# Kernel optimization log

Hardware: AMD Instinct MI355X
Metric: run time of the kernel (lower is better)

## Reference

```python
import jax, jax.numpy as jnp
import numpy as np

EPSILON = 0.3
ALPHA = 0.7
LN_EPS = 1e-5


def _layernorm(x, g, b):
    mu = jnp.mean(x, axis=-1, keepdims=True)
    var = jnp.mean((x - mu) ** 2, axis=-1, keepdims=True)
    return (x - mu) / jnp.sqrt(var + LN_EPS) * g + b


def setup_inputs() -> dict:
    key = jax.random.key(0)
    ks = jax.random.split(key, 6)
    B, N, D, L = 1, 2048, 768, 16
    s = 0.05  # weight scale to keep sigmoid/exp well-conditioned
    return {
        "x": jax.random.normal(ks[0], (B, N, D), jnp.float32),
        "proj_w": jax.random.normal(ks[1], (D, L), jnp.float32) * s,
        "proj_b": jnp.zeros((L,), jnp.float32),
        "ln1_g": jnp.ones((L,), jnp.float32),
        "ln1_b": jnp.zeros((L,), jnp.float32),
        "pi_w1": jax.random.normal(ks[2], (L, D), jnp.float32) * s,
        "pi_b1": jnp.zeros((D,), jnp.float32),
        "pi_w2": jax.random.normal(ks[3], (D, 1), jnp.float32) * s,
        "pi_b2": jnp.zeros((1,), jnp.float32),
        "dt": jnp.full((1,), 0.05, jnp.float32),
        "f_w": jax.random.normal(ks[4], (D, D), jnp.float32) * s,
        "f_b": jnp.zeros((D,), jnp.float32),
        "ln2_g": jnp.ones((D,), jnp.float32),
        "ln2_b": jnp.zeros((D,), jnp.float32),
    }


def reference(x, proj_w, proj_b, ln1_g, ln1_b, pi_w1, pi_b1, pi_w2, pi_b2, dt, f_w, f_b, ln2_g, ln2_b):
    B, N, D = x.shape
    # proj_list: Linear -> LayerNorm -> ReLU. [B,N,L]
    x_proj = jax.nn.relu(_layernorm(x @ proj_w + proj_b, ln1_g, ln1_b))
    # RBF kernel over pairwise differences. [B,N,N]
    diff = x_proj[:, :, None, :] - x_proj[:, None, :, :]
    K_eps = jnp.exp(-(1.0 / (4.0 * EPSILON)) * jnp.sum(diff * diff, axis=-1))
    q_tilde = jnp.sum(K_eps, axis=2)  # [B,N]
    # pi_list: Linear -> ReLU -> Linear -> Sigmoid. [B,N]
    pi = jax.nn.sigmoid(jax.nn.relu(x_proj @ pi_w1 + pi_b1) @ pi_w2 + pi_b2)[..., 0]
    v = pi / q_tilde  # diagonal of D_epsilon_tilde
    # K_tilde = K_eps @ diag(v): column scaling (math-equivalent to bmm with diag_embed)
    K_tilde = K_eps * v[:, None, :]
    d = jnp.sum(K_tilde, axis=2) + 1e-5  # diagonal of D_tilde
    # inv(D_tilde) @ K_tilde: row scaling; then subtract identity
    L_op = (1.0 / EPSILON) * (K_tilde / d[:, :, None]) - jnp.eye(N, dtype=x.dtype)[None]
    L_mat = L_op[0]  # .squeeze(0), B == 1
    # f(x): modeled as linear map
    target = x @ f_w + f_b  # [B,N,D]
    tt = dt * jnp.einsum('ij,bjd->bid', L_mat, target)  # target_transformed
    target1 = target + tt
    target2 = ALPHA * x + (1.0 - ALPHA) * (target1 + tt)
    return _layernorm(target2, ln2_g, ln2_b)
```

## Files before the change

### kernel.cpp

```cpp
#include <hip/hip_runtime.h>
#include <math.h>

#define EPSILON 0.3f
#define ALPHA 0.7f
#define LN_EPS 1e-5f

typedef __bf16 bf16x8 __attribute__((ext_vector_type(8)));
typedef float f32x4 __attribute__((ext_vector_type(4)));

__device__ __forceinline__ unsigned short f2bf(float f) {
  unsigned int u = __float_as_uint(f);
  return (unsigned short)((u + 0x7fffu + ((u >> 16) & 1u)) >> 16);
}
__device__ __forceinline__ unsigned int pack2(float lo, float hi) {
  return (unsigned int)f2bf(lo) | ((unsigned int)f2bf(hi) << 16);
}

__device__ __forceinline__ float wave_reduce(float v) {
#pragma unroll
  for (int off = 32; off > 0; off >>= 1) v += __shfl_xor(v, off, 64);
  return v;
}

__device__ __forceinline__ float blk_reduce_sum(float v, float* red) {
  v = wave_reduce(v);
  int lane = threadIdx.x & 63, wid = threadIdx.x >> 6;
  __syncthreads();
  if (lane == 0) red[wid] = v;
  __syncthreads();
  float s = 0.f;
  int nw = (blockDim.x + 63) >> 6;
  for (int w = 0; w < nw; ++w) s += red[w];
  return s;
}

__global__ __launch_bounds__(256) void k_proj(
    const float* __restrict__ x, const float* __restrict__ proj_w,
    const float* __restrict__ proj_b, const float* __restrict__ ln1_g,
    const float* __restrict__ ln1_b, const float* __restrict__ pi_w1,
    const float* __restrict__ pi_b1, const float* __restrict__ pi_w2,
    const float* __restrict__ pi_b2, float* __restrict__ xp,
    float* __restrict__ s, float* __restrict__ pi, int N, int D) {
  __shared__ float xs[16][68];
  __shared__ float ws[64][20];
  __shared__ float ysh[16][17];
  __shared__ float xps[16][16];
  __shared__ float pr[16][4];
  int tid = threadIdx.x;
  int row0 = blockIdx.x * 16;
  int row = tid >> 4, l = tid & 15;
  int lane = tid & 63, w = tid >> 6;
  int skc = (tid & 15) * 4;
  int wk = tid >> 2, wl = (tid & 3) * 4;
  float acc = 0.f;
  for (int k0 = 0; k0 < D; k0 += 64) {
    float4 xv = *(const float4*)(x + (size_t)(row0 + row) * D + k0 + skc);
    float4 wv = *(const float4*)(proj_w + (size_t)(k0 + wk) * 16 + wl);
    __syncthreads();
    *(float4*)&xs[row][skc] = xv;
    *(float4*)&ws[wk][wl] = wv;
    __syncthreads();
#pragma unroll
    for (int kk = 0; kk < 64; kk += 4) {
      float4 a4 = *(const float4*)&xs[row][kk];
      acc += a4.x * ws[kk + 0][l];
      acc += a4.y * ws[kk + 1][l];
      acc += a4.z * ws[kk + 2][l];
      acc += a4.w * ws[kk + 3][l];
    }
  }
  float y = acc + proj_b[l];
  ysh[row][l] = y;
  __syncthreads();
  float mu = 0.f;
#pragma unroll
  for (int t = 0; t < 16; ++t) mu += ysh[row][t];
  mu *= (1.f / 16.f);
  float var = 0.f;
#pragma unroll
  for (int t = 0; t < 16; ++t) { float d2 = ysh[row][t] - mu; var += d2 * d2; }
  var *= (1.f / 16.f);
  float rstd = rsqrtf(var + LN_EPS);
  float xpv = fmaxf((y - mu) * rstd * ln1_g[l] + ln1_b[l], 0.f);
  xps[row][l] = xpv;
  xp[(size_t)(row0 + row) * 16 + l] = xpv;
  float sq = xpv * xpv;
  sq += __shfl_xor(sq, 8, 64);
  sq += __shfl_xor(sq, 4, 64);
  sq += __shfl_xor(sq, 2, 64);
  sq += __shfl_xor(sq, 1, 64);
  if ((lane & 15) == 0) s[row0 + row] = sq;
  __syncthreads();
  float w1r[3][16], b1r[3], w2r[3];
#pragma unroll
  for (int c = 0; c < 3; ++c) {
    int d0 = tid + c * 256;
    b1r[c] = pi_b1[d0];
    w2r[c] = pi_w2[d0];
#pragma unroll
    for (int t = 0; t < 16; ++t) w1r[c][t] = pi_w1[(size_t)t * D + d0];
  }
  float pacc[16];
#pragma unroll
  for (int r = 0; r < 16; ++r) pacc[r] = 0.f;
#pragma unroll
  for (int r = 0; r < 16; ++r) {
    float xv[16];
#pragma unroll
    for (int t4 = 0; t4 < 4; ++t4) {
      float4 xq = *(const float4*)&xps[r][t4 * 4];
      xv[t4 * 4 + 0] = xq.x; xv[t4 * 4 + 1] = xq.y;
      xv[t4 * 4 + 2] = xq.z; xv[t4 * 4 + 3] = xq.w;
    }
    float pa = 0.f;
#pragma unroll
    for (int c = 0; c < 3; ++c) {
      float h = b1r[c];
#pragma unroll
      for (int t = 0; t < 16; ++t) h += xv[t] * w1r[c][t];
      h = fmaxf(h, 0.f);
      pa += h * w2r[c];
    }
    pacc[r] = pa;
  }
#pragma unroll
  for (int r = 0; r < 16; ++r) {
    float pv = wave_reduce(pacc[r]);
    if (lane == 0) pr[r][w] = pv;
  }
  __syncthreads();
  if (tid < 16) {
    float tot = pr[tid][0] + pr[tid][1] + pr[tid][2] + pr[tid][3] + pi_b2[0];
    pi[row0 + tid] = 1.f / (1.f + expf(-tot));
  }
}

__global__ __launch_bounds__(256) void k_keps(
    const float* __restrict__ xp, const float* __restrict__ s,
    const float* __restrict__ pi, unsigned short* __restrict__ Kb,
    float* __restrict__ q, float* __restrict__ v, int N) {
  __shared__ float qs[4][4];
  int i0 = blockIdx.x * 4;
  int tid = threadIdx.x, lane = tid & 63, w = tid >> 6;
  float a[4][16], si[4];
#pragma unroll
  for (int r = 0; r < 4; ++r) {
    const float* ap = xp + (size_t)(i0 + r) * 16;
#pragma unroll
    for (int t = 0; t < 16; ++t) a[r][t] = ap[t];
    si[r] = s[i0 + r];
  }
  const float c = 1.f / (4.f * EPSILON);
  float qa[4] = {0.f, 0.f, 0.f, 0.f};
  for (int it = 0; it < N / 512; ++it) {
    int j = it * 512 + tid * 2;
    const float4* bp = (const float4*)(xp + (size_t)j * 16);
    float4 b0 = bp[0], b1 = bp[1], b2 = bp[2], b3 = bp[3];
    float4 c0 = bp[4], c1 = bp[5], c2 = bp[6], c3 = bp[7];
    float bv[16] = {b0.x, b0.y, b0.z, b0.w, b1.x, b1.y, b1.z, b1.w,
                    b2.x, b2.y, b2.z, b2.w, b3.x, b3.y, b3.z, b3.w};
    float cv[16] = {c0.x, c0.y, c0.z, c0.w, c1.x, c1.y, c1.z, c1.w,
                    c2.x, c2.y, c2.z, c2.w, c3.x, c3.y, c3.z, c3.w};
    float sj0 = s[j], sj1 = s[j + 1];
#pragma unroll
    for (int r = 0; r < 4; ++r) {
      float d0 = 0.f, d1 = 0.f;
#pragma unroll
      for (int t = 0; t < 16; ++t) { d0 += a[r][t] * bv[t]; d1 += a[r][t] * cv[t]; }
      float k0 = expf(-c * (si[r] + sj0 - 2.f * d0));
      float k1 = expf(-c * (si[r] + sj1 - 2.f * d1));
      *(unsigned int*)(Kb + (size_t)(i0 + r) * N + j) = pack2(k0, k1);
      qa[r] += k0 + k1;
    }
  }
#pragma unroll
  for (int r = 0; r < 4; ++r) {
    float t = wave_reduce(qa[r]);
    if (lane == 0) qs[r][w] = t;
  }
  __syncthreads();
  if (tid < 4) {
    float tot = qs[tid][0] + qs[tid][1] + qs[tid][2] + qs[tid][3];
    q[i0 + tid] = tot;
    v[i0 + tid] = pi[i0 + tid] / tot;
  }
}

__global__ __launch_bounds__(256) void k_prep(
    const unsigned short* __restrict__ Kb, const float* __restrict__ v,
    float* __restrict__ dv, const float* __restrict__ x,
    unsigned short* __restrict__ xvbT, const float* __restrict__ fw,
    unsigned short* __restrict__ fwTb, int N, int D) {
  __shared__ float sh[544];
  int bid = blockIdx.x, tid = threadIdx.x;
  int xvtCols = D / 32;
  int xvtB = xvtCols * (N / 32);
  if (bid < N) {
    int i = bid;
    float acc = 0.f;
    int j8 = tid * 8;
    for (; j8 < N; j8 += 256 * 8) {
      uint4 kv4 = *(const uint4*)(Kb + (size_t)i * N + j8);
      float4 va = *(const float4*)(v + j8);
      float4 vb = *(const float4*)(v + j8 + 4);
      unsigned int u;
      u = kv4.x;
      acc += __uint_as_float(u << 16) * va.x + __uint_as_float(u & 0xffff0000u) * va.y;
      u = kv4.y;
      acc += __uint_as_float(u << 16) * va.z + __uint_as_float(u & 0xffff0000u) * va.w;
      u = kv4.z;
      acc += __uint_as_float(u << 16) * vb.x + __uint_as_float(u & 0xffff0000u) * vb.y;
      u = kv4.w;
      acc += __uint_as_float(u << 16) * vb.z + __uint_as_float(u & 0xffff0000u) * vb.w;
    }
    float tot = blk_reduce_sum(acc, sh);
    if (tid == 0) dv[i] = tot + 1e-5f;
  } else if (bid < N + xvtB) {
    int t = bid - N;
    unsigned short (*tile)[33] = (unsigned short (*)[33])sh;
    int tx = tid & 31, ty = tid >> 5;
    int c0 = (t % xvtCols) * 32;
    int r0 = (t / xvtCols) * 32;
#pragma unroll
    for (int i = 0; i < 4; ++i) {
      int r = r0 + ty + i * 8;
      tile[ty + i * 8][tx] = f2bf(v[r] * x[(size_t)r * D + c0 + tx]);
    }
    __syncthreads();
#pragma unroll
    for (int i = 0; i < 4; ++i) {
      int cc = c0 + ty + i * 8;
      xvbT[(size_t)cc * N + r0 + tx] = tile[tx][ty + i * 8];
    }
  } else {
    int t = bid - N - xvtB;
    unsigned short (*tile)[33] = (unsigned short (*)[33])sh;
    int tx = tid & 31, ty = tid >> 5;
    int tcvtCols = D / 32;
    int c0 = (t % tcvtCols) * 32;
    int r0 = (t / tcvtCols) * 32;
#pragma unroll
    for (int i = 0; i < 4; ++i) {
      int r = r0 + ty + i * 8;
      tile[ty + i * 8][tx] = f2bf(fw[(size_t)r * D + c0 + tx]);
    }
    __syncthreads();
#pragma unroll
    for (int i = 0; i < 4; ++i) {
      int cc = c0 + ty + i * 8;
      fwTb[(size_t)cc * D + r0 + tx] = tile[tx][ty + i * 8];
    }
  }
}

__global__ __launch_bounds__(256) void k_gemmA(
    const unsigned short* __restrict__ A, const unsigned short* __restrict__ Bt,
    const float* __restrict__ x, const float* __restrict__ dv,
    const float* __restrict__ dtp, unsigned short* __restrict__ Z,
    int M, int N, int K) {
  __shared__ unsigned short As[64][72];
  __shared__ unsigned short Bs[64][72];
  int tid = threadIdx.x;
  int w = tid >> 6, l = tid & 63;
  int ln = l & 15, quad = l >> 4;
  int mh = (w & 1) * 32, nh = (w >> 1) * 32;
  int row0 = blockIdx.y * 64, col0 = blockIdx.x * 64;
  int lr = tid >> 3, lc = (tid & 7) * 8;
  f32x4 acc[2][2] = {};
  for (int k0 = 0; k0 < K; k0 += 64) {
    uint4 a0 = *(const uint4*)(A + (size_t)(row0 + lr) * K + k0 + lc);
    uint4 a1 = *(const uint4*)(A + (size_t)(row0 + lr + 32) * K + k0 + lc);
    uint4 b0 = *(const uint4*)(Bt + (size_t)(col0 + lr) * K + k0 + lc);
    uint4 b1 = *(const uint4*)(Bt + (size_t)(col0 + lr + 32) * K + k0 + lc);
    __syncthreads();
    *(uint4*)&As[lr][lc] = a0;
    *(uint4*)&As[lr + 32][lc] = a1;
    *(uint4*)&Bs[lr][lc] = b0;
    *(uint4*)&Bs[lr + 32][lc] = b1;
    __syncthreads();
#pragma unroll
    for (int kss = 0; kss < 2; ++kss) {
      bf16x8 bfr[2], afr[2];
#pragma unroll
      for (int nt = 0; nt < 2; ++nt)
        bfr[nt] = *(const bf16x8*)&Bs[nh + nt * 16 + ln][kss * 32 + quad * 8];
#pragma unroll
      for (int mt = 0; mt < 2; ++mt)
        afr[mt] = *(const bf16x8*)&As[mh + mt * 16 + ln][kss * 32 + quad * 8];
#pragma unroll
      for (int mt = 0; mt < 2; ++mt)
#pragma unroll
        for (int nt = 0; nt < 2; ++nt)
          acc[mt][nt] = __builtin_amdgcn_mfma_f32_16x16x32_bf16(
              afr[mt], bfr[nt], acc[mt][nt], 0, 0, 0);
    }
  }
  float dtv = dtp[0];
  float c2 = (1.f - ALPHA) * (1.f - 2.f * dtv);
  float c3b = (1.f - ALPHA) * 2.f * dtv / EPSILON;
#pragma unroll
  for (int mt = 0; mt < 2; ++mt)
#pragma unroll
    for (int nt = 0; nt < 2; ++nt) {
      int col = col0 + nh + nt * 16 + ln;
#pragma unroll
      for (int r = 0; r < 4; ++r) {
        int row = row0 + mh + mt * 16 + quad * 4 + r;
        float c3 = c3b / dv[row];
        Z[(size_t)row * N + col] =
            f2bf(c2 * x[(size_t)row * N + col] + c3 * acc[mt][nt][r]);
      }
    }
}

__global__ __launch_bounds__(256) void k_gemmB(
    const unsigned short* __restrict__ A, const unsigned short* __restrict__ Bt,
    const float* __restrict__ x, const float* __restrict__ bias,
    const float* __restrict__ dtp, float* __restrict__ out,
    int M, int N, int K) {
  __shared__ unsigned short As[64][72];
  __shared__ unsigned short Bs[64][72];
  int tid = threadIdx.x;
  int w = tid >> 6, l = tid & 63;
  int ln = l & 15, quad = l >> 4;
  int mh = (w & 1) * 32, nh = (w >> 1) * 32;
  int row0 = blockIdx.y * 64, col0 = blockIdx.x * 64;
  int lr = tid >> 3, lc = (tid & 7) * 8;
  f32x4 acc[2][2] = {};
  for (int k0 = 0; k0 < K; k0 += 64) {
    uint4 a0 = *(const uint4*)(A + (size_t)(row0 + lr) * K + k0 + lc);
    uint4 a1 = *(const uint4*)(A + (size_t)(row0 + lr + 32) * K + k0 + lc);
    uint4 b0 = *(const uint4*)(Bt + (size_t)(col0 + lr) * K + k0 + lc);
    uint4 b1 = *(const uint4*)(Bt + (size_t)(col0 + lr + 32) * K + k0 + lc);
    __syncthreads();
    *(uint4*)&As[lr][lc] = a0;
    *(uint4*)&As[lr + 32][lc] = a1;
    *(uint4*)&Bs[lr][lc] = b0;
    *(uint4*)&Bs[lr + 32][lc] = b1;
    __syncthreads();
#pragma unroll
    for (int kss = 0; kss < 2; ++kss) {
      bf16x8 bfr[2], afr[2];
#pragma unroll
      for (int nt = 0; nt < 2; ++nt)
        bfr[nt] = *(const bf16x8*)&Bs[nh + nt * 16 + ln][kss * 32 + quad * 8];
#pragma unroll
      for (int mt = 0; mt < 2; ++mt)
        afr[mt] = *(const bf16x8*)&As[mh + mt * 16 + ln][kss * 32 + quad * 8];
#pragma unroll
      for (int mt = 0; mt < 2; ++mt)
#pragma unroll
        for (int nt = 0; nt < 2; ++nt)
          acc[mt][nt] = __builtin_amdgcn_mfma_f32_16x16x32_bf16(
              afr[mt], bfr[nt], acc[mt][nt], 0, 0, 0);
    }
  }
  float dtv = dtp[0];
  float cb = (1.f - ALPHA) * (1.f - 2.f * dtv) +
             (1.f - ALPHA) * 2.f * dtv / EPSILON;
#pragma unroll
  for (int mt = 0; mt < 2; ++mt)
#pragma unroll
    for (int nt = 0; nt < 2; ++nt) {
      int col = col0 + nh + nt * 16 + ln;
      float bv = cb * bias[col];
#pragma unroll
      for (int r = 0; r < 4; ++r) {
        int row = row0 + mh + mt * 16 + quad * 4 + r;
        size_t idx = (size_t)row * N + col;
        out[idx] = ALPHA * x[idx] + acc[mt][nt][r] + bv;
      }
    }
}

__global__ __launch_bounds__(256) void k_ln_rows(
    float* __restrict__ out, const float* __restrict__ g,
    const float* __restrict__ b, int D) {
  __shared__ float red[4];
  int i = blockIdx.x, tid = threadIdx.x;
  float vv[4];
  int nt = D / 256;
  float sum = 0.f;
  for (int t = 0; t < nt; ++t) {
    vv[t] = out[(size_t)i * D + tid + t * 256];
    sum += vv[t];
  }
  float mu = blk_reduce_sum(sum, red) / (float)D;
  float sq = 0.f;
  for (int t = 0; t < nt; ++t) { float d2 = vv[t] - mu; sq += d2 * d2; }
  float var = blk_reduce_sum(sq, red) / (float)D;
  float rs = rsqrtf(var + LN_EPS);
  for (int t = 0; t < nt; ++t) {
    int d0 = tid + t * 256;
    out[(size_t)i * D + d0] = (vv[t] - mu) * rs * g[d0] + b[d0];
  }
}

extern "C" void kernel_launch(void* const* d_in, const int* in_sizes, int n_in,
                              void* d_out, int out_size, void* d_ws, size_t ws_size,
                              hipStream_t stream) {
  const float* x = (const float*)d_in[0];
  const float* proj_w = (const float*)d_in[1];
  const float* proj_b = (const float*)d_in[2];
  const float* ln1_g = (const float*)d_in[3];
  const float* ln1_b = (const float*)d_in[4];
  const float* pi_w1 = (const float*)d_in[5];
  const float* pi_b1 = (const float*)d_in[6];
  const float* pi_w2 = (const float*)d_in[7];
  const float* pi_b2 = (const float*)d_in[8];
  const float* dt = (const float*)d_in[9];
  const float* f_w = (const float*)d_in[10];
  const float* f_b = (const float*)d_in[11];
  const float* ln2_g = (const float*)d_in[12];
  const float* ln2_b = (const float*)d_in[13];
  float* out = (float*)d_out;

  int D = in_sizes[11];
  int N = in_sizes[0] / D;

  unsigned short* Kb = (unsigned short*)d_ws;
  unsigned short* xvbT = Kb + (size_t)N * N;
  unsigned short* fwTb = xvbT + (size_t)D * N;
  unsigned short* Z = fwTb + (size_t)D * D;
  float* xp = (float*)(Z + (size_t)N * D);
  float* s = xp + (size_t)N * 16;
  float* pi = s + N;
  float* q = pi + N;
  float* v = q + N;
  float* dv = v + N;

  int xvtB = (D / 32) * (N / 32);
  int tcvtB = (D / 32) * (D / 32);

  k_proj<<<N / 16, 256, 0, stream>>>(x, proj_w, proj_b, ln1_g, ln1_b, pi_w1,
                                     pi_b1, pi_w2, pi_b2, xp, s, pi, N, D);
  k_keps<<<N / 4, 256, 0, stream>>>(xp, s, pi, Kb, q, v, N);
  k_prep<<<N + xvtB + tcvtB, 256, 0, stream>>>(Kb, v, dv, x, xvbT, f_w, fwTb,
                                               N, D);
  k_gemmA<<<dim3(D / 64, N / 64), 256, 0, stream>>>(Kb, xvbT, x, dv, dt, Z,
                                                    N, D, N);
  k_gemmB<<<dim3(D / 64, N / 64), 256, 0, stream>>>(Z, fwTb, x, f_b, dt, out,
                                                    N, D, D);
  k_ln_rows<<<N, 256, 0, stream>>>(out, ln2_g, ln2_b, D);
}
```

Measured before the change: 161.4 us.

## Use direct global-to-LDS loads with XOR swizzle in GEMMs; move fw transpose into proj

Both MFMA GEMM kernels now stage tiles with global_load_lds (16-byte direct-to-LDS loads) into an unpadded XOR-swizzled shared layout, instead of loading to registers and then storing to padded LDS. The goal is to cut register round-trips and LDS store instructions while avoiding bank conflicts through the swizzle. The f_w transpose/convert blocks move from k_prep into extra blocks of k_proj, so that work overlaps with the small projection kernel. The unused q buffer is dropped. The K loop still has no double buffering, so load latency stays exposed at every barrier.

```diff
diff --git a/kernel.cpp b/kernel.cpp
--- a/kernel.cpp
+++ b/kernel.cpp
@@ -14,6 +14,13 @@
 }
 __device__ __forceinline__ unsigned int pack2(float lo, float hi) {
   return (unsigned int)f2bf(lo) | ((unsigned int)f2bf(hi) << 16);
+}
+
+__device__ __forceinline__ void async16(const unsigned short* g,
+                                        unsigned short* l) {
+  __builtin_amdgcn_global_load_lds(
+      (const __attribute__((address_space(1))) unsigned int*)g,
+      (__attribute__((address_space(3))) unsigned int*)l, 16, 0, 0);
 }
 
 __device__ __forceinline__ float wave_reduce(float v) {
@@ -39,7 +46,8 @@
     const float* __restrict__ proj_b, const float* __restrict__ ln1_g,
     const float* __restrict__ ln1_b, const float* __restrict__ pi_w1,
     const float* __restrict__ pi_b1, const float* __restrict__ pi_w2,
-    const float* __restrict__ pi_b2, float* __restrict__ xp,
+    const float* __restrict__ pi_b2, const float* __restrict__ fw,
+    unsigned short* __restrict__ fwTb, float* __restrict__ xp,
     float* __restrict__ s, float* __restrict__ pi, int N, int D) {
   __shared__ float xs[16][68];
   __shared__ float ws[64][20];
@@ -47,6 +55,26 @@
   __shared__ float xps[16][16];
   __shared__ float pr[16][4];
   int tid = threadIdx.x;
+  int nProj = N / 16;
+  if (blockIdx.x >= (unsigned)nProj) {
+    unsigned short(*tile)[33] = (unsigned short(*)[33])&ws[0][0];
+    int t = blockIdx.x - nProj;
+    int tx = tid & 31, ty = tid >> 5;
+    int cols = D / 32;
+    int c0 = (t % cols) * 32, r0 = (t / cols) * 32;
+#pragma unroll
+    for (int i = 0; i < 4; ++i) {
+      int r = r0 + ty + i * 8;
+      tile[ty + i * 8][tx] = f2bf(fw[(size_t)r * D + c0 + tx]);
+    }
+    __syncthreads();
+#pragma unroll
+    for (int i = 0; i < 4; ++i) {
+      int cc = c0 + ty + i * 8;
+      fwTb[(size_t)cc * D + r0 + tx] = tile[tx][ty + i * 8];
+    }
+    return;
+  }
   int row0 = blockIdx.x * 16;
   int row = tid >> 4, l = tid & 15;
   int lane = tid & 63, w = tid >> 6;
@@ -138,7 +166,7 @@
 __global__ __launch_bounds__(256) void k_keps(
     const float* __restrict__ xp, const float* __restrict__ s,
     const float* __restrict__ pi, unsigned short* __restrict__ Kb,
-    float* __restrict__ q, float* __restrict__ v, int N) {
+    float* __restrict__ v, int N) {
   __shared__ float qs[4][4];
   int i0 = blockIdx.x * 4;
   int tid = threadIdx.x, lane = tid & 63, w = tid >> 6;
@@ -181,7 +209,6 @@
   __syncthreads();
   if (tid < 4) {
     float tot = qs[tid][0] + qs[tid][1] + qs[tid][2] + qs[tid][3];
-    q[i0 + tid] = tot;
     v[i0 + tid] = pi[i0 + tid] / tot;
   }
 }
@@ -189,17 +216,13 @@
 __global__ __launch_bounds__(256) void k_prep(
     const unsigned short* __restrict__ Kb, const float* __restrict__ v,
     float* __restrict__ dv, const float* __restrict__ x,
-    unsigned short* __restrict__ xvbT, const float* __restrict__ fw,
-    unsigned short* __restrict__ fwTb, int N, int D) {
+    unsigned short* __restrict__ xvbT, int N, int D) {
   __shared__ float sh[544];
   int bid = blockIdx.x, tid = threadIdx.x;
-  int xvtCols = D / 32;
-  int xvtB = xvtCols * (N / 32);
   if (bid < N) {
     int i = bid;
     float acc = 0.f;
-    int j8 = tid * 8;
-    for (; j8 < N; j8 += 256 * 8) {
+    for (int j8 = tid * 8; j8 < N; j8 += 256 * 8) {
       uint4 kv4 = *(const uint4*)(Kb + (size_t)i * N + j8);
       float4 va = *(const float4*)(v + j8);
       float4 vb = *(const float4*)(v + j8 + 4);
@@ -215,12 +238,13 @@
     }
     float tot = blk_reduce_sum(acc, sh);
     if (tid == 0) dv[i] = tot + 1e-5f;
-  } else if (bid < N + xvtB) {
+  } else {
     int t = bid - N;
-    unsigned short (*tile)[33] = (unsigned short (*)[33])sh;
+    unsigned short(*tile)[33] = (unsigned short(*)[33])sh;
     int tx = tid & 31, ty = tid >> 5;
-    int c0 = (t % xvtCols) * 32;
-    int r0 = (t / xvtCols) * 32;
+    int cols = D / 32;
+    int c0 = (t % cols) * 32;
+    int r0 = (t / cols) * 32;
 #pragma unroll
     for (int i = 0; i < 4; ++i) {
       int r = r0 + ty + i * 8;
@@ -232,69 +256,65 @@
       int cc = c0 + ty + i * 8;
       xvbT[(size_t)cc * N + r0 + tx] = tile[tx][ty + i * 8];
     }
-  } else {
-    int t = bid - N - xvtB;
-    unsigned short (*tile)[33] = (unsigned short (*)[33])sh;
-    int tx = tid & 31, ty = tid >> 5;
-    int tcvtCols = D / 32;
-    int c0 = (t % tcvtCols) * 32;
-    int r0 = (t / tcvtCols) * 32;
-#pragma unroll
-    for (int i = 0; i < 4; ++i) {
-      int r = r0 + ty + i * 8;
-      tile[ty + i * 8][tx] = f2bf(fw[(size_t)r * D + c0 + tx]);
-    }
-    __syncthreads();
-#pragma unroll
-    for (int i = 0; i < 4; ++i) {
-      int cc = c0 + ty + i * 8;
-      fwTb[(size_t)cc * D + r0 + tx] = tile[tx][ty + i * 8];
-    }
-  }
-}
+  }
+}
+
+#define GEMM_KLOOP(Aptr, Bptr, Kdim)                                          \
+  int tid = threadIdx.x;                                                      \
+  int w = tid >> 6, l = tid & 63;                                             \
+  int ln = l & 15, quad = l >> 4;                                             \
+  int mh = (w & 1) * 32, nh = (w >> 1) * 32;                                  \
+  int row0 = blockIdx.y * 64, col0 = blockIdx.x * 64;                         \
+  int sr = l >> 3, sj = l & 7;                                                \
+  int swz = (sj ^ sr) * 8;                                                    \
+  const unsigned short* gA0 = Aptr + (size_t)(row0 + w * 8 + sr) * Kdim + swz;\
+  const unsigned short* gB0 = Bptr + (size_t)(col0 + w * 8 + sr) * Kdim + swz;\
+  const unsigned short* gA1 = gA0 + (size_t)32 * Kdim;                        \
+  const unsigned short* gB1 = gB0 + (size_t)32 * Kdim;                        \
+  unsigned short* lA0 = As + w * 8 * 64;                                      \
+  unsigned short* lA1 = As + (32 + w * 8) * 64;                               \
+  unsigned short* lB0 = Bs + w * 8 * 64;                                      \
+  unsigned short* lB1 = Bs + (32 + w * 8) * 64;                               \
+  f32x4 acc[2][2] = {};                                                       \
+  for (int k0 = 0; k0 < Kdim; k0 += 64) {                                     \
+    __syncthreads();                                                          \
+    async16(gA0 + k0, lA0);                                                   \
+    async16(gA1 + k0, lA1);                                                   \
+    async16(gB0 + k0, lB0);                                                   \
+    async16(gB1 + k0, lB1);                                                   \
+    __syncthreads();                                                          \
+    _Pragma("unroll")                                                         \
+    for (int ks = 0; ks < 2; ++ks) {                                          \
+      bf16x8 bfr[2], afr[2];                                                  \
+      _Pragma("unroll")                                                       \
+      for (int nt = 0; nt < 2; ++nt) {                                        \
+        int r = nh + nt * 16 + ln;                                            \
+        int cix = (ks * 4 + quad) ^ (r & 7);                                  \
+        bfr[nt] = *(const bf16x8*)&Bs[r * 64 + cix * 8];                      \
+      }                                                                       \
+      _Pragma("unroll")                                                       \
+      for (int mt = 0; mt < 2; ++mt) {                                        \
+        int r = mh + mt * 16 + ln;                                            \
+        int cix = (ks * 4 + quad) ^ (r & 7);                                  \
+        afr[mt] = *(const bf16x8*)&As[r * 64 + cix * 8];                      \
+      }                                                                       \
+      _Pragma("unroll")                                                       \
+      for (int mt = 0; mt < 2; ++mt)                                          \
+        _Pragma("unroll")                                                     \
+        for (int nt = 0; nt < 2; ++nt)                                        \
+          acc[mt][nt] = __builtin_amdgcn_mfma_f32_16x16x32_bf16(              \
+              afr[mt], bfr[nt], acc[mt][nt], 0, 0, 0);                        \
+    }                                                                         \
+  }
 
 __global__ __launch_bounds__(256) void k_gemmA(
     const unsigned short* __restrict__ A, const unsigned short* __restrict__ Bt,
     const float* __restrict__ x, const float* __restrict__ dv,
     const float* __restrict__ dtp, unsigned short* __restrict__ Z,
     int M, int N, int K) {
-  __shared__ unsigned short As[64][72];
-  __shared__ unsigned short Bs[64][72];
-  int tid = threadIdx.x;
-  int w = tid >> 6, l = tid & 63;
-  int ln = l & 15, quad = l >> 4;
-  int mh = (w & 1) * 32, nh = (w >> 1) * 32;
-  int row0 = blockIdx.y * 64, col0 = blockIdx.x * 64;
-  int lr = tid >> 3, lc = (tid & 7) * 8;
-  f32x4 acc[2][2] = {};
-  for (int k0 = 0; k0 < K; k0 += 64) {
-    uint4 a0 = *(const uint4*)(A + (size_t)(row0 + lr) * K + k0 + lc);
-    uint4 a1 = *(const uint4*)(A + (size_t)(row0 + lr + 32) * K + k0 + lc);
-    uint4 b0 = *(const uint4*)(Bt + (size_t)(col0 + lr) * K + k0 + lc);
-    uint4 b1 = *(const uint4*)(Bt + (size_t)(col0 + lr + 32) * K + k0 + lc);
-    __syncthreads();
-    *(uint4*)&As[lr][lc] = a0;
-    *(uint4*)&As[lr + 32][lc] = a1;
-    *(uint4*)&Bs[lr][lc] = b0;
-    *(uint4*)&Bs[lr + 32][lc] = b1;
-    __syncthreads();
-#pragma unroll
-    for (int kss = 0; kss < 2; ++kss) {
-      bf16x8 bfr[2], afr[2];
-#pragma unroll
-      for (int nt = 0; nt < 2; ++nt)
-        bfr[nt] = *(const bf16x8*)&Bs[nh + nt * 16 + ln][kss * 32 + quad * 8];
-#pragma unroll
-      for (int mt = 0; mt < 2; ++mt)
-        afr[mt] = *(const bf16x8*)&As[mh + mt * 16 + ln][kss * 32 + quad * 8];
-#pragma unroll
-      for (int mt = 0; mt < 2; ++mt)
-#pragma unroll
-        for (int nt = 0; nt < 2; ++nt)
-          acc[mt][nt] = __builtin_amdgcn_mfma_f32_16x16x32_bf16(
-              afr[mt], bfr[nt], acc[mt][nt], 0, 0, 0);
-    }
-  }
+  __shared__ unsigned short As[64 * 64];
+  __shared__ unsigned short Bs[64 * 64];
+  GEMM_KLOOP(A, Bt, K)
   float dtv = dtp[0];
   float c2 = (1.f - ALPHA) * (1.f - 2.f * dtv);
   float c3b = (1.f - ALPHA) * 2.f * dtv / EPSILON;
@@ -318,43 +338,9 @@
     const float* __restrict__ x, const float* __restrict__ bias,
     const float* __restrict__ dtp, float* __restrict__ out,
     int M, int N, int K) {
-  __shared__ unsigned short As[64][72];
-  __shared__ unsigned short Bs[64][72];
-  int tid = threadIdx.x;
-  int w = tid >> 6, l = tid & 63;
-  int ln = l & 15, quad = l >> 4;
-  int mh = (w & 1) * 32, nh = (w >> 1) * 32;
-  int row0 = blockIdx.y * 64, col0 = blockIdx.x * 64;
-  int lr = tid >> 3, lc = (tid & 7) * 8;
-  f32x4 acc[2][2] = {};
-  for (int k0 = 0; k0 < K; k0 += 64) {
-    uint4 a0 = *(const uint4*)(A + (size_t)(row0 + lr) * K + k0 + lc);
-    uint4 a1 = *(const uint4*)(A + (size_t)(row0 + lr + 32) * K + k0 + lc);
-    uint4 b0 = *(const uint4*)(Bt + (size_t)(col0 + lr) * K + k0 + lc);
-    uint4 b1 = *(const uint4*)(Bt + (size_t)(col0 + lr + 32) * K + k0 + lc);
-    __syncthreads();
-    *(uint4*)&As[lr][lc] = a0;
-    *(uint4*)&As[lr + 32][lc] = a1;
-    *(uint4*)&Bs[lr][lc] = b0;
-    *(uint4*)&Bs[lr + 32][lc] = b1;
-    __syncthreads();
-#pragma unroll
-    for (int kss = 0; kss < 2; ++kss) {
-      bf16x8 bfr[2], afr[2];
-#pragma unroll
-      for (int nt = 0; nt < 2; ++nt)
-        bfr[nt] = *(const bf16x8*)&Bs[nh + nt * 16 + ln][kss * 32 + quad * 8];
-#pragma unroll
-      for (int mt = 0; mt < 2; ++mt)
-        afr[mt] = *(const bf16x8*)&As[mh + mt * 16 + ln][kss * 32 + quad * 8];
-#pragma unroll
-      for (int mt = 0; mt < 2; ++mt)
-#pragma unroll
-        for (int nt = 0; nt < 2; ++nt)
-          acc[mt][nt] = __builtin_amdgcn_mfma_f32_16x16x32_bf16(
-              afr[mt], bfr[nt], acc[mt][nt], 0, 0, 0);
-    }
-  }
+  __shared__ unsigned short As[64 * 64];
+  __shared__ unsigned short Bs[64 * 64];
+  GEMM_KLOOP(A, Bt, K)
   float dtv = dtp[0];
   float cb = (1.f - ALPHA) * (1.f - 2.f * dtv) +
              (1.f - ALPHA) * 2.f * dtv / EPSILON;
@@ -425,18 +411,17 @@
   float* xp = (float*)(Z + (size_t)N * D);
   float* s = xp + (size_t)N * 16;
   float* pi = s + N;
-  float* q = pi + N;
-  float* v = q + N;
+  float* v = pi + N;
   float* dv = v + N;
 
+  int fwB = (D / 32) * (D / 32);
   int xvtB = (D / 32) * (N / 32);
-  int tcvtB = (D / 32) * (D / 32);
-
-  k_proj<<<N / 16, 256, 0, stream>>>(x, proj_w, proj_b, ln1_g, ln1_b, pi_w1,
-                                     pi_b1, pi_w2, pi_b2, xp, s, pi, N, D);
-  k_keps<<<N / 4, 256, 0, stream>>>(xp, s, pi, Kb, q, v, N);
-  k_prep<<<N + xvtB + tcvtB, 256, 0, stream>>>(Kb, v, dv, x, xvbT, f_w, fwTb,
-                                               N, D);
+
+  k_proj<<<N / 16 + fwB, 256, 0, stream>>>(x, proj_w, proj_b, ln1_g, ln1_b,
+                                           pi_w1, pi_b1, pi_w2, pi_b2, f_w,
+                                           fwTb, xp, s, pi, N, D);
+  k_keps<<<N / 4, 256, 0, stream>>>(xp, s, pi, Kb, v, N);
+  k_prep<<<N + xvtB, 256, 0, stream>>>(Kb, v, dv, x, xvbT, N, D);
   k_gemmA<<<dim3(D / 64, N / 64), 256, 0, stream>>>(Kb, xvbT, x, dv, dt, Z,
                                                     N, D, N);
   k_gemmB<<<dim3(D / 64, N / 64), 256, 0, stream>>>(Z, fwTb, x, f_b, dt, out,
```

Result: no change. 159.4 us (-1.3%).

## Fold row-sum into GEMM via MFMA, async LDS loads with swizzle

Applied to the files above, without the earlier changes.

Drops the separate pass that re-read the full N×N bf16 kernel matrix to compute the D_tilde row sums. Those sums are now accumulated inside gemmA as an extra MFMA against the bf16 v vector. The f_w transpose moves into spare k_proj blocks, and v scaling gets its own small kernel. Both GEMMs switch to global_load_lds direct-to-LDS copies with an XOR swizzle instead of register staging and padding, and exp uses __expf. Computing dv from bf16-rounded v changes numerics slightly, and gemmA does extra MFMA work on every tile.

```diff
diff --git a/kernel.cpp b/kernel.cpp
--- a/kernel.cpp
+++ b/kernel.cpp
@@ -12,8 +12,18 @@
   unsigned int u = __float_as_uint(f);
   return (unsigned short)((u + 0x7fffu + ((u >> 16) & 1u)) >> 16);
 }
+__device__ __forceinline__ float bf2f(unsigned short h) {
+  return __uint_as_float(((unsigned int)h) << 16);
+}
 __device__ __forceinline__ unsigned int pack2(float lo, float hi) {
   return (unsigned int)f2bf(lo) | ((unsigned int)f2bf(hi) << 16);
+}
+
+__device__ __forceinline__ void async16(const unsigned short* g,
+                                        unsigned short* l) {
+  __builtin_amdgcn_global_load_lds(
+      (const __attribute__((address_space(1))) unsigned int*)g,
+      (__attribute__((address_space(3))) unsigned int*)l, 16, 0, 0);
 }
 
 __device__ __forceinline__ float wave_reduce(float v) {
@@ -28,10 +38,7 @@
   __syncthreads();
   if (lane == 0) red[wid] = v;
   __syncthreads();
-  float s = 0.f;
-  int nw = (blockDim.x + 63) >> 6;
-  for (int w = 0; w < nw; ++w) s += red[w];
-  return s;
+  return red[0] + red[1] + red[2] + red[3];
 }
 
 __global__ __launch_bounds__(256) void k_proj(
@@ -39,7 +46,8 @@
     const float* __restrict__ proj_b, const float* __restrict__ ln1_g,
     const float* __restrict__ ln1_b, const float* __restrict__ pi_w1,
     const float* __restrict__ pi_b1, const float* __restrict__ pi_w2,
-    const float* __restrict__ pi_b2, float* __restrict__ xp,
+    const float* __restrict__ pi_b2, const float* __restrict__ fw,
+    unsigned short* __restrict__ fwTb, float* __restrict__ xp,
     float* __restrict__ s, float* __restrict__ pi, int N, int D) {
   __shared__ float xs[16][68];
   __shared__ float ws[64][20];
@@ -47,6 +55,26 @@
   __shared__ float xps[16][16];
   __shared__ float pr[16][4];
   int tid = threadIdx.x;
+  int nProj = N / 16;
+  if (blockIdx.x >= (unsigned)nProj) {
+    unsigned short(*tile)[33] = (unsigned short(*)[33])&ws[0][0];
+    int t = blockIdx.x - nProj;
+    int tx = tid & 31, ty = tid >> 5;
+    int cols = D / 32;
+    int c0 = (t % cols) * 32, r0 = (t / cols) * 32;
+#pragma unroll
+    for (int i = 0; i < 4; ++i) {
+      int r = r0 + ty + i * 8;
+      tile[ty + i * 8][tx] = f2bf(fw[(size_t)r * D + c0 + tx]);
+    }
+    __syncthreads();
+#pragma unroll
+    for (int i = 0; i < 4; ++i) {
+      int cc = c0 + ty + i * 8;
+      fwTb[(size_t)cc * D + r0 + tx] = tile[tx][ty + i * 8];
+    }
+    return;
+  }
   int row0 = blockIdx.x * 16;
   int row = tid >> 4, l = tid & 15;
   int lane = tid & 63, w = tid >> 6;
@@ -100,9 +128,6 @@
 #pragma unroll
     for (int t = 0; t < 16; ++t) w1r[c][t] = pi_w1[(size_t)t * D + d0];
   }
-  float pacc[16];
-#pragma unroll
-  for (int r = 0; r < 16; ++r) pacc[r] = 0.f;
 #pragma unroll
   for (int r = 0; r < 16; ++r) {
     float xv[16];
@@ -121,11 +146,7 @@
       h = fmaxf(h, 0.f);
       pa += h * w2r[c];
     }
-    pacc[r] = pa;
-  }
-#pragma unroll
-  for (int r = 0; r < 16; ++r) {
-    float pv = wave_reduce(pacc[r]);
+    float pv = wave_reduce(pa);
     if (lane == 0) pr[r][w] = pv;
   }
   __syncthreads();
@@ -138,7 +159,7 @@
 __global__ __launch_bounds__(256) void k_keps(
     const float* __restrict__ xp, const float* __restrict__ s,
     const float* __restrict__ pi, unsigned short* __restrict__ Kb,
-    float* __restrict__ q, float* __restrict__ v, int N) {
+    unsigned short* __restrict__ vb, int N) {
   __shared__ float qs[4][4];
   int i0 = blockIdx.x * 4;
   int tid = threadIdx.x, lane = tid & 63, w = tid >> 6;
@@ -167,8 +188,8 @@
       float d0 = 0.f, d1 = 0.f;
 #pragma unroll
       for (int t = 0; t < 16; ++t) { d0 += a[r][t] * bv[t]; d1 += a[r][t] * cv[t]; }
-      float k0 = expf(-c * (si[r] + sj0 - 2.f * d0));
-      float k1 = expf(-c * (si[r] + sj1 - 2.f * d1));
+      float k0 = __expf(-c * (si[r] + sj0 - 2.f * d0));
+      float k1 = __expf(-c * (si[r] + sj1 - 2.f * d1));
       *(unsigned int*)(Kb + (size_t)(i0 + r) * N + j) = pack2(k0, k1);
       qa[r] += k0 + k1;
     }
@@ -181,118 +202,84 @@
   __syncthreads();
   if (tid < 4) {
     float tot = qs[tid][0] + qs[tid][1] + qs[tid][2] + qs[tid][3];
-    q[i0 + tid] = tot;
-    v[i0 + tid] = pi[i0 + tid] / tot;
-  }
-}
-
-__global__ __launch_bounds__(256) void k_prep(
-    const unsigned short* __restrict__ Kb, const float* __restrict__ v,
-    float* __restrict__ dv, const float* __restrict__ x,
-    unsigned short* __restrict__ xvbT, const float* __restrict__ fw,
-    unsigned short* __restrict__ fwTb, int N, int D) {
-  __shared__ float sh[544];
-  int bid = blockIdx.x, tid = threadIdx.x;
-  int xvtCols = D / 32;
-  int xvtB = xvtCols * (N / 32);
-  if (bid < N) {
-    int i = bid;
-    float acc = 0.f;
-    int j8 = tid * 8;
-    for (; j8 < N; j8 += 256 * 8) {
-      uint4 kv4 = *(const uint4*)(Kb + (size_t)i * N + j8);
-      float4 va = *(const float4*)(v + j8);
-      float4 vb = *(const float4*)(v + j8 + 4);
-      unsigned int u;
-      u = kv4.x;
-      acc += __uint_as_float(u << 16) * va.x + __uint_as_float(u & 0xffff0000u) * va.y;
-      u = kv4.y;
-      acc += __uint_as_float(u << 16) * va.z + __uint_as_float(u & 0xffff0000u) * va.w;
-      u = kv4.z;
-      acc += __uint_as_float(u << 16) * vb.x + __uint_as_float(u & 0xffff0000u) * vb.y;
-      u = kv4.w;
-      acc += __uint_as_float(u << 16) * vb.z + __uint_as_float(u & 0xffff0000u) * vb.w;
-    }
-    float tot = blk_reduce_sum(acc, sh);
-    if (tid == 0) dv[i] = tot + 1e-5f;
-  } else if (bid < N + xvtB) {
-    int t = bid - N;
-    unsigned short (*tile)[33] = (unsigned short (*)[33])sh;
-    int tx = tid & 31, ty = tid >> 5;
-    int c0 = (t % xvtCols) * 32;
-    int r0 = (t / xvtCols) * 32;
-#pragma unroll
-    for (int i = 0; i < 4; ++i) {
-      int r = r0 + ty + i * 8;
-      tile[ty + i * 8][tx] = f2bf(v[r] * x[(size_t)r * D + c0 + tx]);
-    }
-    __syncthreads();
-#pragma unroll
-    for (int i = 0; i < 4; ++i) {
-      int cc = c0 + ty + i * 8;
-      xvbT[(size_t)cc * N + r0 + tx] = tile[tx][ty + i * 8];
-    }
-  } else {
-    int t = bid - N - xvtB;
-    unsigned short (*tile)[33] = (unsigned short (*)[33])sh;
-    int tx = tid & 31, ty = tid >> 5;
-    int tcvtCols = D / 32;
-    int c0 = (t % tcvtCols) * 32;
-    int r0 = (t / tcvtCols) * 32;
-#pragma unroll
-    for (int i = 0; i < 4; ++i) {
-      int r = r0 + ty + i * 8;
-      tile[ty + i * 8][tx] = f2bf(fw[(size_t)r * D + c0 + tx]);
-    }
-    __syncthreads();
-#pragma unroll
-    for (int i = 0; i < 4; ++i) {
-      int cc = c0 + ty + i * 8;
-      fwTb[(size_t)cc * D + r0 + tx] = tile[tx][ty + i * 8];
-    }
+    vb[i0 + tid] = f2bf(pi[i0 + tid] / tot);
+  }
+}
+
+__global__ __launch_bounds__(256) void k_scale(
+    const float* __restrict__ x, const unsigned short* __restrict__ vb,
+    unsigned short* __restrict__ xvbT, int N, int D) {
+  __shared__ unsigned short tile[32][33];
+  int tid = threadIdx.x;
+  int tx = tid & 31, ty = tid >> 5;
+  int cols = D / 32;
+  int c0 = ((int)blockIdx.x % cols) * 32;
+  int r0 = ((int)blockIdx.x / cols) * 32;
+#pragma unroll
+  for (int i = 0; i < 4; ++i) {
+    int r = r0 + ty + i * 8;
+    tile[ty + i * 8][tx] = f2bf(bf2f(vb[r]) * x[(size_t)r * D + c0 + tx]);
+  }
+  __syncthreads();
+#pragma unroll
+  for (int i = 0; i < 4; ++i) {
+    int cc = c0 + ty + i * 8;
+    xvbT[(size_t)cc * N + r0 + tx] = tile[tx][ty + i * 8];
   }
 }
 
 __global__ __launch_bounds__(256) void k_gemmA(
     const unsigned short* __restrict__ A, const unsigned short* __restrict__ Bt,
-    const float* __restrict__ x, const float* __restrict__ dv,
+    const unsigned short* __restrict__ vb, const float* __restrict__ x,
     const float* __restrict__ dtp, unsigned short* __restrict__ Z,
     int M, int N, int K) {
-  __shared__ unsigned short As[64][72];
-  __shared__ unsigned short Bs[64][72];
+  __shared__ unsigned short As[64 * 64];
+  __shared__ unsigned short Bs[64 * 64];
   int tid = threadIdx.x;
   int w = tid >> 6, l = tid & 63;
   int ln = l & 15, quad = l >> 4;
   int mh = (w & 1) * 32, nh = (w >> 1) * 32;
   int row0 = blockIdx.y * 64, col0 = blockIdx.x * 64;
-  int lr = tid >> 3, lc = (tid & 7) * 8;
+  int sr = l >> 3, sj = l & 7;
+  int swz = (sj ^ sr) * 8;
+  const unsigned short* gA0 = A + (size_t)(row0 + w * 8 + sr) * K + swz;
+  const unsigned short* gB0 = Bt + (size_t)(col0 + w * 8 + sr) * K + swz;
+  const unsigned short* gA1 = gA0 + (size_t)32 * K;
+  const unsigned short* gB1 = gB0 + (size_t)32 * K;
   f32x4 acc[2][2] = {};
+  f32x4 adv[2] = {};
   for (int k0 = 0; k0 < K; k0 += 64) {
-    uint4 a0 = *(const uint4*)(A + (size_t)(row0 + lr) * K + k0 + lc);
-    uint4 a1 = *(const uint4*)(A + (size_t)(row0 + lr + 32) * K + k0 + lc);
-    uint4 b0 = *(const uint4*)(Bt + (size_t)(col0 + lr) * K + k0 + lc);
-    uint4 b1 = *(const uint4*)(Bt + (size_t)(col0 + lr + 32) * K + k0 + lc);
-    __syncthreads();
-    *(uint4*)&As[lr][lc] = a0;
-    *(uint4*)&As[lr + 32][lc] = a1;
-    *(uint4*)&Bs[lr][lc] = b0;
-    *(uint4*)&Bs[lr + 32][lc] = b1;
-    __syncthreads();
-#pragma unroll
-    for (int kss = 0; kss < 2; ++kss) {
+    __syncthreads();
+    async16(gA0 + k0, As + w * 8 * 64);
+    async16(gA1 + k0, As + (32 + w * 8) * 64);
+    async16(gB0 + k0, Bs + w * 8 * 64);
+    async16(gB1 + k0, Bs + (32 + w * 8) * 64);
+    __syncthreads();
+#pragma unroll
+    for (int ks = 0; ks < 2; ++ks) {
       bf16x8 bfr[2], afr[2];
-#pragma unroll
-      for (int nt = 0; nt < 2; ++nt)
-        bfr[nt] = *(const bf16x8*)&Bs[nh + nt * 16 + ln][kss * 32 + quad * 8];
-#pragma unroll
-      for (int mt = 0; mt < 2; ++mt)
-        afr[mt] = *(const bf16x8*)&As[mh + mt * 16 + ln][kss * 32 + quad * 8];
-#pragma unroll
-      for (int mt = 0; mt < 2; ++mt)
+      bf16x8 bvf = *(const bf16x8*)(vb + k0 + ks * 32 + quad * 8);
+#pragma unroll
+      for (int nt = 0; nt < 2; ++nt) {
+        int r = nh + nt * 16 + ln;
+        int cix = (ks * 4 + quad) ^ (r & 7);
+        bfr[nt] = *(const bf16x8*)&Bs[r * 64 + cix * 8];
+      }
+#pragma unroll
+      for (int mt = 0; mt < 2; ++mt) {
+        int r = mh + mt * 16 + ln;
+        int cix = (ks * 4 + quad) ^ (r & 7);
+        afr[mt] = *(const bf16x8*)&As[r * 64 + cix * 8];
+      }
+#pragma unroll
+      for (int mt = 0; mt < 2; ++mt) {
+        adv[mt] = __builtin_amdgcn_mfma_f32_16x16x32_bf16(afr[mt], bvf,
+                                                          adv[mt], 0, 0, 0);
 #pragma unroll
         for (int nt = 0; nt < 2; ++nt)
           acc[mt][nt] = __builtin_amdgcn_mfma_f32_16x16x32_bf16(
               afr[mt], bfr[nt], acc[mt][nt], 0, 0, 0);
+      }
     }
   }
   float dtv = dtp[0];
@@ -306,9 +293,9 @@
 #pragma unroll
       for (int r = 0; r < 4; ++r) {
         int row = row0 + mh + mt * 16 + quad * 4 + r;
-        float c3 = c3b / dv[row];
+        float dvv = adv[mt][r] + 1e-5f;
         Z[(size_t)row * N + col] =
-            f2bf(c2 * x[(size_t)row * N + col] + c3 * acc[mt][nt][r]);
+            f2bf(c2 * x[(size_t)row * N + col] + (c3b / dvv) * acc[mt][nt][r]);
       }
     }
 }
@@ -318,35 +305,42 @@
     const float* __restrict__ x, const float* __restrict__ bias,
     const float* __restrict__ dtp, float* __restrict__ out,
     int M, int N, int K) {
-  __shared__ unsigned short As[64][72];
-  __shared__ unsigned short Bs[64][72];
+  __shared__ unsigned short As[64 * 64];
+  __shared__ unsigned short Bs[64 * 64];
   int tid = threadIdx.x;
   int w = tid >> 6, l = tid & 63;
   int ln = l & 15, quad = l >> 4;
   int mh = (w & 1) * 32, nh = (w >> 1) * 32;
   int row0 = blockIdx.y * 64, col0 = blockIdx.x * 64;
-  int lr = tid >> 3, lc = (tid & 7) * 8;
+  int sr = l >> 3, sj = l & 7;
+  int swz = (sj ^ sr) * 8;
+  const unsigned short* gA0 = A + (size_t)(row0 + w * 8 + sr) * K + swz;
+  const unsigned short* gB0 = Bt + (size_t)(col0 + w * 8 + sr) * K + swz;
+  const unsigned short* gA1 = gA0 + (size_t)32 * K;
+  const unsigned short* gB1 = gB0 + (size_t)32 * K;
   f32x4 acc[2][2] = {};
   for (int k0 = 0; k0 < K; k0 += 64) {
-    uint4 a0 = *(const uint4*)(A + (size_t)(row0 + lr) * K + k0 + lc);
-    uint4 a1 = *(const uint4*)(A + (size_t)(row0 + lr + 32) * K + k0 + lc);
-    uint4 b0 = *(const uint4*)(Bt + (size_t)(col0 + lr) * K + k0 + lc);
-    uint4 b1 = *(const uint4*)(Bt + (size_t)(col0 + lr + 32) * K + k0 + lc);
-    __syncthreads();
-    *(uint4*)&As[lr][lc] = a0;
-    *(uint4*)&As[lr + 32][lc] = a1;
-    *(uint4*)&Bs[lr][lc] = b0;
-    *(uint4*)&Bs[lr + 32][lc] = b1;
-    __syncthreads();
-#pragma unroll
-    for (int kss = 0; kss < 2; ++kss) {
+    __syncthreads();
+    async16(gA0 + k0, As + w * 8 * 64);
+    async16(gA1 + k0, As + (32 + w * 8) * 64);
+    async16(gB0 + k0, Bs + w * 8 * 64);
+    async16(gB1 + k0, Bs + (32 + w * 8) * 64);
+    __syncthreads();
+#pragma unroll
+    for (int ks = 0; ks < 2; ++ks) {
       bf16x8 bfr[2], afr[2];
 #pragma unroll
-      for (int nt = 0; nt < 2; ++nt)
-        bfr[nt] = *(const bf16x8*)&Bs[nh + nt * 16 + ln][kss * 32 + quad * 8];
-#pragma unroll
-      for (int mt = 0; mt < 2; ++mt)
-        afr[mt] = *(const bf16x8*)&As[mh + mt * 16 + ln][kss * 32 + quad * 8];
+      for (int nt = 0; nt < 2; ++nt) {
+        int r = nh + nt * 16 + ln;
+        int cix = (ks * 4 + quad) ^ (r & 7);
+        bfr[nt] = *(const bf16x8*)&Bs[r * 64 + cix * 8];
+      }
+#pragma unroll
+      for (int mt = 0; mt < 2; ++mt) {
+        int r = mh + mt * 16 + ln;
+        int cix = (ks * 4 + quad) ^ (r & 7);
+        afr[mt] = *(const bf16x8*)&As[r * 64 + cix * 8];
+      }
 #pragma unroll
       for (int mt = 0; mt < 2; ++mt)
 #pragma unroll
@@ -422,22 +416,19 @@
   unsigned short* xvbT = Kb + (size_t)N * N;
   unsigned short* fwTb = xvbT + (size_t)D * N;
   unsigned short* Z = fwTb + (size_t)D * D;
-  float* xp = (float*)(Z + (size_t)N * D);
+  unsigned short* vb = Z + (size_t)N * D;
+  float* xp = (float*)(vb + N);
   float* s = xp + (size_t)N * 16;
   float* pi = s + N;
-  float* q = pi + N;
-  float* v = q + N;
-  float* dv = v + N;
-
-  int xvtB = (D / 32) * (N / 32);
-  int tcvtB = (D / 32) * (D / 32);
-
-  k_proj<<<N / 16, 256, 0, stream>>>(x, proj_w, proj_b, ln1_g, ln1_b, pi_w1,
-                                     pi_b1, pi_w2, pi_b2, xp, s, pi, N, D);
-  k_keps<<<N / 4, 256, 0, stream>>>(xp, s, pi, Kb, q, v, N);
-  k_prep<<<N + xvtB + tcvtB, 256, 0, stream>>>(Kb, v, dv, x, xvbT, f_w, fwTb,
-                                               N, D);
-  k_gemmA<<<dim3(D / 64, N / 64), 256, 0, stream>>>(Kb, xvbT, x, dv, dt, Z,
+
+  int fwB = (D / 32) * (D / 32);
+
+  k_proj<<<N / 16 + fwB, 256, 0, stream>>>(x, proj_w, proj_b, ln1_g, ln1_b,
+                                           pi_w1, pi_b1, pi_w2, pi_b2, f_w,
+                                           fwTb, xp, s, pi, N, D);
+  k_keps<<<N / 4, 256, 0, stream>>>(xp, s, pi, Kb, vb, N);
+  k_scale<<<(N / 32) * (D / 32), 256, 0, stream>>>(x, vb, xvbT, N, D);
+  k_gemmA<<<dim3(D / 64, N / 64), 256, 0, stream>>>(Kb, xvbT, vb, x, dt, Z,
                                                     N, D, N);
   k_gemmB<<<dim3(D / 64, N / 64), 256, 0, stream>>>(Z, fwTb, x, f_b, dt, out,
                                                     N, D, D);
```

Result: slower. 171.9 us (+6.5%).
